# Kernel optimization log

Hardware: AMD Instinct MI355X
Metric: run time of the kernel (lower is better)

## Reference

```python
import jax, jax.numpy as jnp
import numpy as np

T, XDIM, ZDIM = 500000, 64, 64


def setup_inputs() -> dict:
    key = jax.random.key(0)
    ks = jax.random.split(key, 6)
    return {
        "X_t": jax.random.normal(ks[0], (T, XDIM), dtype=jnp.float32),
        "Z_t": jax.random.normal(ks[1], (T, ZDIM), dtype=jnp.float32),
        "G": jax.random.uniform(ks[2], (), dtype=jnp.float32),
        "eta": jax.random.normal(ks[3], (XDIM,), dtype=jnp.float32),
        "zeta": jax.random.normal(ks[4], (ZDIM,), dtype=jnp.float32),
        "gamma": jax.random.normal(ks[5], (ZDIM,), dtype=jnp.float32),
    }


def reference(X_t, Z_t, G, eta, zeta, gamma):
    # theta_t = sigmoid(G) * theta_{t-1} + dot(Z[t-1], gamma), theta_0 = 0
    # Y_t = theta_t + dot(X[t], eta) + dot(Z[t], zeta)
    G_hat = jax.nn.sigmoid(G)  # addSigmoid=True path
    c = Z_t @ gamma                                   # [T]
    u = jnp.concatenate([jnp.zeros((1,), c.dtype), c[:-1]])  # shifted drive, u_0 = 0
    a = jnp.full_like(u, G_hat)

    def combine(x, y):
        a1, b1 = x
        a2, b2 = y
        return a1 * a2, b1 * a2 + b2

    _, theta = jax.lax.associative_scan(combine, (a, u))  # [T], theta_0 = 0
    return theta + X_t @ eta + Z_t @ zeta
```

## Files before the change

kernel.cpp:

```cpp
#include <hip/hip_runtime.h>


#define WIN    64
#define CHUNK  256

template <int N>
__device__ __forceinline__ float rshr_add(float v) {
    const int s = __builtin_amdgcn_update_dpp(
        0, __float_as_int(v), 0x110 | N , 0xF, 0xF, true);
    return v + __int_as_float(s);
}
__device__ __forceinline__ float rsum16(float v) {
    v = rshr_add<8>(v);
    v = rshr_add<4>(v);
    v = rshr_add<2>(v);
    v = rshr_add<1>(v);
    return v;
}

__global__ __launch_bounds__(256) void dlm_pass1(
    const float* __restrict__ X, const float* __restrict__ Z,
    const float* __restrict__ eta, const float* __restrict__ zeta,
    const float* __restrict__ gam,
    float* __restrict__ c_ws, float* __restrict__ b_out, int T)
{
    const int tid  = threadIdx.x;
    const int lane = tid & 63;
    const int wv   = tid >> 6;
    const int sub  = lane & 15;
    const int rsub = lane >> 4;
    const int s    = (int)blockIdx.x * CHUNK;
    const int Tm1  = T - 1;

    __shared__ float cl[CHUNK];
    __shared__ float bl[CHUNK];

    const float4 e4  = ((const float4*)eta)[sub];
    const float4 sz4 = ((const float4*)zeta)[sub];
    const float4 g4  = ((const float4*)gam)[sub];
    const float4* X4 = (const float4*)X;
    const float4* Z4 = (const float4*)Z;

    float4 zzA[4], xxA[4], zzB[4], xxB[4];

    auto issue = [&](float4 (&zb)[4], float4 (&xb)[4], int i) {
        const int rb = s + i * 64 + wv * 16;
        #pragma unroll
        for (int u = 0; u < 4; ++u) {
            const int    r = min(rb + u * 4 + rsub, Tm1);
            const size_t o = (size_t)r * 16 + sub;
            zb[u] = Z4[o];
            xb[u] = X4[o];
        }
    };

    auto reduce_store = [&](const float4 (&zb)[4], const float4 (&xb)[4], int i) {
        float cp[4], bp[4];
        #pragma unroll
        for (int u = 0; u < 4; ++u) {
            const float4 z = zb[u], x = xb[u];
            cp[u] = z.x*g4.x + z.y*g4.y + z.z*g4.z + z.w*g4.w;
            bp[u] = x.x*e4.x + x.y*e4.y + x.z*e4.z + x.w*e4.w
                  + z.x*sz4.x + z.y*sz4.y + z.z*sz4.z + z.w*sz4.w;
            cp[u] = rsum16(cp[u]);
            bp[u] = rsum16(bp[u]);
        }
        if (sub == 15) {
            #pragma unroll
            for (int u = 0; u < 4; ++u) {
                const int idx = i * 64 + wv * 16 + u * 4 + rsub;
                cl[idx] = cp[u];
                bl[idx] = bp[u];
            }
        }
    };

    issue(zzA, xxA, 0);
    issue(zzB, xxB, 1);
    reduce_store(zzA, xxA, 0);
    issue(zzA, xxA, 2);
    reduce_store(zzB, xxB, 1);
    issue(zzB, xxB, 3);
    reduce_store(zzA, xxA, 2);
    reduce_store(zzB, xxB, 3);

    __syncthreads();

    const int t = s + tid;
    if (t < T) {
        c_ws[t]  = cl[tid];
        b_out[t] = bl[tid];
    }
}

__global__ __launch_bounds__(256) void dlm_pass2(
    const float* __restrict__ c, const float* __restrict__ Gp,
    float* __restrict__ out, int T)
{
    const int tid = threadIdx.x;
    const int s   = (int)blockIdx.x * CHUNK;
    const int t   = s + tid;

    __shared__ float sc[CHUNK];
    __shared__ float theta_sh;

    const float g   = *Gp;
    const float a   = 1.0f / (1.0f + expf(-g));
    const float l2a = log2f(a);

    const float v = (t >= 1 && t < T) ? c[t - 1] : 0.0f;
    const float b = (t < T) ? out[t] : 0.0f;

    if (tid < 64) {
        float term = 0.0f;
        const int idx = s - 2 - tid;
        if (tid <= WIN - 2 && idx >= 0)
            term = exp2f((float)tid * l2a) * c[idx];
        #pragma unroll
        for (int off = 1; off <= 32; off <<= 1)
            term += __shfl_xor(term, off, 64);
        if (tid == 0) theta_sh = term;
    }

    sc[tid] = v;
    __syncthreads();
    const float theta_in = theta_sh;

    float Ad = a;
    for (int d = 1; d < CHUNK; d <<= 1) {
        const float self = sc[tid];
        const float prev = (tid >= d) ? sc[tid - d] : 0.0f;
        __syncthreads();
        sc[tid] = self + Ad * prev;
        __syncthreads();
        Ad *= Ad;
    }

    const float E = (tid > 0) ? sc[tid - 1] : 0.0f;
    float theta = exp2f((float)tid * l2a) * theta_in + E;
    theta = a * theta + v;
    if (t < T) out[t] = b + theta;
}

#define RPI    64
#define NITER  ((WIN + CHUNK) / RPI)

__global__ __launch_bounds__(256) void dlm_fused(
    const float* __restrict__ X, const float* __restrict__ Z,
    const float* __restrict__ Gp,
    const float* __restrict__ eta, const float* __restrict__ zeta,
    const float* __restrict__ gam,
    float* __restrict__ out, int T)
{
    const int tid  = threadIdx.x;
    const int lane = tid & 63;
    const int wv   = tid >> 6;
    const int sub  = lane & 15;
    const int rsub = lane >> 4;
    const int s    = (int)blockIdx.x * CHUNK;

    __shared__ float cl[WIN + CHUNK];
    __shared__ float bl[CHUNK];
    __shared__ float sc[256];
    __shared__ float theta_sh;

    const float4 e4  = ((const float4*)eta)[sub];
    const float4 sz4 = ((const float4*)zeta)[sub];
    const float4 g4  = ((const float4*)gam)[sub];
    const float4* X4 = (const float4*)X;
    const float4* Z4 = (const float4*)Z;

    const float g   = *Gp;
    const float a   = 1.0f / (1.0f + expf(-g));
    const float l2a = log2f(a);

    for (int i = 0; i < NITER; ++i) {
        const int rb = s - WIN + i * RPI + wv * 16;
        float cp[4], bp[4];
        #pragma unroll
        for (int u = 0; u < 4; ++u) {
            const int r = rb + u * 4 + rsub;
            float4 z = make_float4(0.f, 0.f, 0.f, 0.f);
            float4 x = make_float4(0.f, 0.f, 0.f, 0.f);
            const bool in = (r >= 0) && (r < T);
            if (in)           z = Z4[(size_t)r * 16 + sub];
            if (in && i > 0)  x = X4[(size_t)r * 16 + sub];
            cp[u] = z.x*g4.x + z.y*g4.y + z.z*g4.z + z.w*g4.w;
            bp[u] = x.x*e4.x + x.y*e4.y + x.z*e4.z + x.w*e4.w
                  + z.x*sz4.x + z.y*sz4.y + z.z*sz4.z + z.w*sz4.w;
        }
        #pragma unroll
        for (int u = 0; u < 4; ++u) {
            #pragma unroll
            for (int off = 1; off <= 8; off <<= 1) {
                cp[u] += __shfl_xor(cp[u], off, 64);
                bp[u] += __shfl_xor(bp[u], off, 64);
            }
        }
        if (sub == 0) {
            #pragma unroll
            for (int u = 0; u < 4; ++u) {
                const int r = rb + u * 4 + rsub;
                cl[r - s + WIN] = cp[u];
                if (i > 0) bl[r - s] = bp[u];
            }
        }
    }
    __syncthreads();

    if (tid < 64) {
        float term = 0.0f;
        if (tid <= WIN - 2)
            term = exp2f((float)tid * l2a) * cl[WIN - 2 - tid];
        #pragma unroll
        for (int off = 1; off <= 32; off <<= 1)
            term += __shfl_xor(term, off, 64);
        if (tid == 0) theta_sh = term;
    }

    const int t = s + tid;
    const float v = (t == 0) ? 0.0f : cl[WIN + tid - 1];
    sc[tid] = v;
    __syncthreads();
    const float theta_in = theta_sh;

    float Ad = a;
    for (int d = 1; d < 256; d <<= 1) {
        const float self = sc[tid];
        const float prev = (tid >= d) ? sc[tid - d] : 0.0f;
        __syncthreads();
        sc[tid] = self + Ad * prev;
        __syncthreads();
        Ad *= Ad;
    }

    const float E = (tid > 0) ? sc[tid - 1] : 0.0f;
    float theta = exp2f((float)tid * l2a) * theta_in + E;
    theta = a * theta + v;
    if (t < T) out[t] = bl[tid] + theta;
}

extern "C" void kernel_launch(void* const* d_in, const int* in_sizes, int n_in,
                              void* d_out, int out_size, void* d_ws, size_t ws_size,
                              hipStream_t stream) {
    const float* X     = (const float*)d_in[0];
    const float* Z     = (const float*)d_in[1];
    const float* G     = (const float*)d_in[2];
    const float* eta   = (const float*)d_in[3];
    const float* zeta  = (const float*)d_in[4];
    const float* gamma = (const float*)d_in[5];
    float* out = (float*)d_out;

    const int T = in_sizes[0] / 64;
    const int nblk = (T + CHUNK - 1) / CHUNK;

    if (ws_size >= (size_t)T * sizeof(float)) {
        float* c_ws = (float*)d_ws;
        dlm_pass1<<<nblk, 256, 0, stream>>>(X, Z, eta, zeta, gamma, c_ws, out, T);
        dlm_pass2<<<nblk, 256, 0, stream>>>(c_ws, G, out, T);
    } else {
        dlm_fused<<<nblk, 256, 0, stream>>>(X, Z, G, eta, zeta, gamma, out, T);
    }
}
```

Baseline: 276.3 us.

## Stage pass1 X/Z tiles through LDS via direct global-to-LDS loads

Pass1 now uses global_load_lds to copy a 128-row tile of Z and X straight into shared memory with an XOR swizzle, then reads float4s from LDS for the dot-product reductions. Chunk size for pass1 drops to 128 rows so the tile fits (64 KB of LDS per block), and pass2 and the fused kernel get their own chunk constants. Results are written directly from lane 15 instead of going through an LDS staging array. The aim is deeper memory-level parallelism from asynchronous bulk loads, at the cost of high LDS use that limits blocks per CU and a full-tile wait before any compute.

Result: no change. 277.3 us (+0.3%).

```diff
diff --git a/kernel.cpp b/kernel.cpp
--- a/kernel.cpp
+++ b/kernel.cpp
@@ -1,8 +1,12 @@
 #include <hip/hip_runtime.h>
 
 
-#define WIN    64
-#define CHUNK  256
+#define WIN     64
+#define CHUNK   128
+#define P2C     256
+#define FCHUNK  256
+#define RPI     64
+#define NITER   ((WIN + FCHUNK) / RPI)
 
 template <int N>
 __device__ __forceinline__ float rshr_add(float v) {
@@ -16,6 +20,12 @@
     v = rshr_add<2>(v);
     v = rshr_add<1>(v);
     return v;
+}
+
+__device__ __forceinline__ void gload16(const float* g, float* l) {
+    __builtin_amdgcn_global_load_lds(
+        (const __attribute__((address_space(1))) void*)g,
+        (__attribute__((address_space(3))) void*)l, 16, 0, 0);
 }
 
 __global__ __launch_bounds__(256) void dlm_pass1(
@@ -32,64 +42,45 @@
     const int s    = (int)blockIdx.x * CHUNK;
     const int Tm1  = T - 1;
 
-    __shared__ float cl[CHUNK];
-    __shared__ float bl[CHUNK];
+    __shared__ __align__(16) float zl[CHUNK * 64];
+    __shared__ __align__(16) float xl[CHUNK * 64];
 
     const float4 e4  = ((const float4*)eta)[sub];
     const float4 sz4 = ((const float4*)zeta)[sub];
     const float4 g4  = ((const float4*)gam)[sub];
-    const float4* X4 = (const float4*)X;
-    const float4* Z4 = (const float4*)Z;
-
-    float4 zzA[4], xxA[4], zzB[4], xxB[4];
-
-    auto issue = [&](float4 (&zb)[4], float4 (&xb)[4], int i) {
-        const int rb = s + i * 64 + wv * 16;
+
+    #pragma unroll
+    for (int j = 0; j < 8; ++j) {
+        const int rb = wv * 32 + j * 4;
+        const int r  = rb + (lane >> 4);
+        const int gr = min(s + r, Tm1);
+        const int gs = (lane & 15) ^ (r & 7);
+        const size_t o = (size_t)gr * 64 + gs * 4;
+        gload16(Z + o, &zl[rb * 64]);
+        gload16(X + o, &xl[rb * 64]);
+    }
+    asm volatile("s_waitcnt vmcnt(0)" ::: "memory");
+    __syncthreads();
+
+    #pragma unroll
+    for (int i = 0; i < CHUNK / 64; ++i) {
         #pragma unroll
         for (int u = 0; u < 4; ++u) {
-            const int    r = min(rb + u * 4 + rsub, Tm1);
-            const size_t o = (size_t)r * 16 + sub;
-            zb[u] = Z4[o];
-            xb[u] = X4[o];
-        }
-    };
-
-    auto reduce_store = [&](const float4 (&zb)[4], const float4 (&xb)[4], int i) {
-        float cp[4], bp[4];
-        #pragma unroll
-        for (int u = 0; u < 4; ++u) {
-            const float4 z = zb[u], x = xb[u];
-            cp[u] = z.x*g4.x + z.y*g4.y + z.z*g4.z + z.w*g4.w;
-            bp[u] = x.x*e4.x + x.y*e4.y + x.z*e4.z + x.w*e4.w
-                  + z.x*sz4.x + z.y*sz4.y + z.z*sz4.z + z.w*sz4.w;
-            cp[u] = rsum16(cp[u]);
-            bp[u] = rsum16(bp[u]);
-        }
-        if (sub == 15) {
-            #pragma unroll
-            for (int u = 0; u < 4; ++u) {
-                const int idx = i * 64 + wv * 16 + u * 4 + rsub;
-                cl[idx] = cp[u];
-                bl[idx] = bp[u];
+            const int ri = i * 64 + wv * 16 + u * 4 + rsub;
+            const int sl = ((sub ^ (ri & 7)) << 2);
+            const float4 z = *(const float4*)&zl[ri * 64 + sl];
+            const float4 x = *(const float4*)&xl[ri * 64 + sl];
+            float cp = z.x*g4.x + z.y*g4.y + z.z*g4.z + z.w*g4.w;
+            float bp = x.x*e4.x + x.y*e4.y + x.z*e4.z + x.w*e4.w
+                     + z.x*sz4.x + z.y*sz4.y + z.z*sz4.z + z.w*sz4.w;
+            cp = rsum16(cp);
+            bp = rsum16(bp);
+            const int t = s + ri;
+            if (sub == 15 && t < T) {
+                c_ws[t]  = cp;
+                b_out[t] = bp;
             }
         }
-    };
-
-    issue(zzA, xxA, 0);
-    issue(zzB, xxB, 1);
-    reduce_store(zzA, xxA, 0);
-    issue(zzA, xxA, 2);
-    reduce_store(zzB, xxB, 1);
-    issue(zzB, xxB, 3);
-    reduce_store(zzA, xxA, 2);
-    reduce_store(zzB, xxB, 3);
-
-    __syncthreads();
-
-    const int t = s + tid;
-    if (t < T) {
-        c_ws[t]  = cl[tid];
-        b_out[t] = bl[tid];
     }
 }
 
@@ -98,10 +89,10 @@
     float* __restrict__ out, int T)
 {
     const int tid = threadIdx.x;
-    const int s   = (int)blockIdx.x * CHUNK;
+    const int s   = (int)blockIdx.x * P2C;
     const int t   = s + tid;
 
-    __shared__ float sc[CHUNK];
+    __shared__ float sc[P2C];
     __shared__ float theta_sh;
 
     const float g   = *Gp;
@@ -127,7 +118,7 @@
     const float theta_in = theta_sh;
 
     float Ad = a;
-    for (int d = 1; d < CHUNK; d <<= 1) {
+    for (int d = 1; d < P2C; d <<= 1) {
         const float self = sc[tid];
         const float prev = (tid >= d) ? sc[tid - d] : 0.0f;
         __syncthreads();
@@ -141,9 +132,6 @@
     theta = a * theta + v;
     if (t < T) out[t] = b + theta;
 }
-
-#define RPI    64
-#define NITER  ((WIN + CHUNK) / RPI)
 
 __global__ __launch_bounds__(256) void dlm_fused(
     const float* __restrict__ X, const float* __restrict__ Z,
@@ -157,10 +145,10 @@
     const int wv   = tid >> 6;
     const int sub  = lane & 15;
     const int rsub = lane >> 4;
-    const int s    = (int)blockIdx.x * CHUNK;
-
-    __shared__ float cl[WIN + CHUNK];
-    __shared__ float bl[CHUNK];
+    const int s    = (int)blockIdx.x * FCHUNK;
+
+    __shared__ float cl[WIN + FCHUNK];
+    __shared__ float bl[FCHUNK];
     __shared__ float sc[256];
     __shared__ float theta_sh;
 
@@ -252,13 +240,15 @@
     float* out = (float*)d_out;
 
     const int T = in_sizes[0] / 64;
-    const int nblk = (T + CHUNK - 1) / CHUNK;
 
     if (ws_size >= (size_t)T * sizeof(float)) {
         float* c_ws = (float*)d_ws;
-        dlm_pass1<<<nblk, 256, 0, stream>>>(X, Z, eta, zeta, gamma, c_ws, out, T);
-        dlm_pass2<<<nblk, 256, 0, stream>>>(c_ws, G, out, T);
+        const int nb1 = (T + CHUNK - 1) / CHUNK;
+        const int nb2 = (T + P2C - 1) / P2C;
+        dlm_pass1<<<nb1, 256, 0, stream>>>(X, Z, eta, zeta, gamma, c_ws, out, T);
+        dlm_pass2<<<nb2, 256, 0, stream>>>(c_ws, G, out, T);
     } else {
-        dlm_fused<<<nblk, 256, 0, stream>>>(X, Z, G, eta, zeta, gamma, out, T);
-    }
-}
+        const int nbf = (T + FCHUNK - 1) / FCHUNK;
+        dlm_fused<<<nbf, 256, 0, stream>>>(X, Z, G, eta, zeta, gamma, out, T);
+    }
+}
```
